# Kernel optimization log

Measured on AMD Instinct MI355X. Metric: run time of the kernel, lower is better.

Reference implementation:

```python
import jax, jax.numpy as jnp
import numpy as np

B, M, N = 2, 256, 256
K, P, Q, D = 8, 512, 512, 64
R, Pp, Qp, Dp = 128, 512, 512, 64
TEMP = float(np.sqrt(Dp))  # softmax temperature = sqrt(D')


def _xavier(key, shape):
    # xavier_uniform over last two dims (fan_in, fan_out), matching torch init on (K, d, D)
    fan_in, fan_out = shape[-2], shape[-1]
    lim = float(np.sqrt(6.0 / (fan_in + fan_out)))
    return jax.random.uniform(key, shape, jnp.float32, -lim, lim)


def setup_inputs() -> dict:
    key = jax.random.key(0)
    ks = jax.random.split(key, 9)
    return {
        "z": jax.random.normal(ks[0], (B, M, N, R), jnp.float32),
        "y_q": jax.random.normal(ks[1], (B, N, Qp), jnp.float32),
        "x_k": jax.random.normal(ks[2], (B, M, Pp), jnp.float32),
        "Theta_x": _xavier(ks[3], (K, P, D)),
        "Theta_y": _xavier(ks[4], (K, Q, D)),
        "Lam_x": _xavier(ks[5], (K, Pp, Dp)),
        "Lam_y": _xavier(ks[6], (K, Qp, Dp)),
        "Lam_zx": _xavier(ks[7], (K, R, Dp)),
        "Lam_zy": _xavier(ks[8], (K, R, Dp)),
    }


def reference(z, y_q, x_k, Theta_x, Theta_y, Lam_x, Lam_y, Lam_zx, Lam_zy):
    # --- mixed attention scores ---
    xt = jnp.einsum('bmp,kpd->bkmd', x_k, Lam_x)          # [B,K,M,D']
    yt = jnp.einsum('bnq,kqd->bknd', y_q, Lam_y)          # [B,K,N,D']
    r = jnp.einsum('bkmd,bknd->bkmn', xt, yt)             # pairwise term
    zy = jnp.einsum('bmnr,krd->bkmnd', z, Lam_zy)         # [B,K,M,N,D'] (large)
    r = r + jnp.einsum('bkmnd,bkmd->bkmn', zy, xt)
    r = r + jnp.einsum('bknd,bmnr,krd->bkmn', yt, z, Lam_zx)
    # --- generalised convolution (mask=None, bias=False) ---
    a = jax.nn.softmax(r / TEMP, axis=-2)                 # softmax over M (column-wise)
    xv = jnp.einsum('bmp,kpd->bkmd', x_k, Theta_x)        # value projection
    y = jnp.einsum('bkmn,bkmd,kqd->bnq', a, xv, Theta_y)  # [B,N,Q]
    return y
```

## Files before the change

### kernel.cpp

```cpp
#include <hip/hip_runtime.h>
#include <hip/hip_bf16.h>

#define LOG2E_OVER_T 0.18033688011112042f

typedef __attribute__((ext_vector_type(8))) short short8;
typedef __attribute__((ext_vector_type(4))) float f32x4;
typedef unsigned short ushort_t;
typedef unsigned long long ull_t;

#define MFMA16(a, b, c) __builtin_amdgcn_mfma_f32_16x16x32_bf16(a, b, c, 0, 0, 0)

__device__ __forceinline__ ushort_t f2bf(float f) {
    union { float f; unsigned u; } v; v.f = f;
    unsigned r = (v.u + 0x7fffu + ((v.u >> 16) & 1u)) >> 16;
    return (ushort_t)r;
}

__device__ __forceinline__ void split8(const float4 a, const float4 b,
                                       short8& hi, short8& lo)
{
    union { float f[8]; unsigned u[8]; } Z;
    Z.f[0] = a.x; Z.f[1] = a.y; Z.f[2] = a.z; Z.f[3] = a.w;
    Z.f[4] = b.x; Z.f[5] = b.y; Z.f[6] = b.z; Z.f[7] = b.w;
    union { unsigned u[4]; short8 s; } H, L;
    #pragma unroll
    for (int i = 0; i < 4; i++) {
        const unsigned u0 = Z.u[2 * i], u1 = Z.u[2 * i + 1];
        H.u[i] = __builtin_amdgcn_perm(u1, u0, 0x07060302u);
        union { unsigned u; float f; } h0, h1;
        h0.u = u0 & 0xffff0000u; h1.u = u1 & 0xffff0000u;
        union { float f; unsigned u; } l0, l1;
        l0.f = Z.f[2 * i] - h0.f; l1.f = Z.f[2 * i + 1] - h1.f;
        L.u[i] = __builtin_amdgcn_perm(l1.u, l0.u, 0x07060302u);
    }
    hi = H.s; lo = L.s;
}

__device__ __forceinline__ void mfma_core64(
    const ushort_t* __restrict__ Ag, int lda,
    const ushort_t* __restrict__ Btg, int ldb,
    int ksteps, f32x4 acc[2][2])
{
    __shared__ __align__(16) ushort_t As[64 * 40];
    __shared__ __align__(16) ushort_t Bs[64 * 40];
    const int t = threadIdx.x;
    const int srow = t >> 2, skc = (t & 3) * 8;
    const int lane = t & 63, w = t >> 6;
    const int wr = w >> 1, wc = w & 1;
    const int fr = lane & 15, kg = lane >> 4;
    const int aoff = (wr * 32 + fr) * 40 + kg * 8;
    const int boff = (wc * 32 + fr) * 40 + kg * 8;
    const long arow = (long)srow * lda + skc;
    const long brow = (long)srow * ldb + skc;

    short8 ra = *(const short8*)(Ag + arow);
    short8 rb = *(const short8*)(Btg + brow);
    for (int kt = 0; kt < ksteps; kt++) {
        __syncthreads();
        *(short8*)&As[srow * 40 + skc] = ra;
        *(short8*)&Bs[srow * 40 + skc] = rb;
        __syncthreads();
        if (kt + 1 < ksteps) {
            ra = *(const short8*)(Ag + arow + (kt + 1) * 32);
            rb = *(const short8*)(Btg + brow + (kt + 1) * 32);
        }
        short8 a0 = *(const short8*)&As[aoff];
        short8 a1 = *(const short8*)&As[aoff + 16 * 40];
        short8 b0 = *(const short8*)&Bs[boff];
        short8 b1 = *(const short8*)&Bs[boff + 16 * 40];
        acc[0][0] = MFMA16(a0, b0, acc[0][0]);
        acc[0][1] = MFMA16(a0, b1, acc[0][1]);
        acc[1][0] = MFMA16(a1, b0, acc[1][0]);
        acc[1][1] = MFMA16(a1, b1, acc[1][1]);
    }
}

__device__ __forceinline__ void zero_acc(f32x4 acc[2][2]) {
    const f32x4 z4 = {0.f, 0.f, 0.f, 0.f};
    acc[0][0] = z4; acc[0][1] = z4; acc[1][0] = z4; acc[1][1] = z4;
}

__global__ __launch_bounds__(256)
void convert_kernel(const float* __restrict__ x_k, const float* __restrict__ y_q,
                    const float* __restrict__ Lam_x, const float* __restrict__ Theta_x,
                    const float* __restrict__ Lam_y, const float* __restrict__ Lam_zy,
                    const float* __restrict__ Lam_zx, const float* __restrict__ Theta_y,
                    ushort_t* __restrict__ xkb, ushort_t* __restrict__ yqb,
                    ushort_t* __restrict__ WxTb, ushort_t* __restrict__ WyTb,
                    ushort_t* __restrict__ Zyb, ushort_t* __restrict__ Zxb,
                    ushort_t* __restrict__ TyTb, float* __restrict__ ssum)
{
    int i = blockIdx.x * 256 + threadIdx.x;
    if (i < 262144) { xkb[i] = f2bf(x_k[i]); return; }
    i -= 262144;
    if (i < 262144) { yqb[i] = f2bf(y_q[i]); return; }
    i -= 262144;
    if (i < 524288) {
        const int k = i >> 16, rem = i & 65535, dc = rem >> 9, p = i & 511;
        const float v = (dc < 64) ? Lam_x[((long)k * 512 + p) * 64 + dc]
                                  : Theta_x[((long)k * 512 + p) * 64 + dc - 64];
        WxTb[i] = f2bf(v); return;
    }
    i -= 524288;
    if (i < 262144) {
        const int k = i >> 15, d = (i >> 9) & 63, p = i & 511;
        WyTb[i] = f2bf(Lam_y[((long)k * 512 + p) * 64 + d]); return;
    }
    i -= 262144;
    if (i < 65536) { Zyb[i] = f2bf(Lam_zy[i]); return; }
    i -= 65536;
    if (i < 65536) { Zxb[i] = f2bf(Lam_zx[i]); return; }
    i -= 65536;
    if (i < 262144) {
        const int q = i >> 9, kd = i & 511, k = kd >> 6, d = kd & 63;
        TyTb[i] = f2bf(Theta_y[((long)k * 512 + q) * 64 + d]); return;
    }
    i -= 262144;
    ssum[i] = 0.f;
}

__global__ __launch_bounds__(256)
void proj_kernel(const ushort_t* __restrict__ xkb, const ushort_t* __restrict__ yqb,
                 const ushort_t* __restrict__ WxTb, const ushort_t* __restrict__ WyTb,
                 ushort_t* __restrict__ xtb, ushort_t* __restrict__ ytb,
                 ushort_t* __restrict__ xvTb)
{
    const int side = blockIdx.z;
    const int bx = blockIdx.x, by = blockIdx.y;
    if (side == 1 && bx >= 8) return;
    f32x4 acc[2][2]; zero_acc(acc);
    const int t = threadIdx.x, lane = t & 63, w = t >> 6;
    const int wr = w >> 1, wc = w & 1, fr = lane & 15, kg = lane >> 4;

    if (side == 0) {
        mfma_core64(xkb + (long)(by * 64) * 512, 512,
                    WxTb + (long)(bx * 64) * 512, 512, 16, acc);
        const int k = bx >> 1, isxv = bx & 1;
        #pragma unroll
        for (int mi = 0; mi < 2; mi++)
        #pragma unroll
        for (int ni = 0; ni < 2; ni++) {
            const int grow0 = by * 64 + wr * 32 + mi * 16 + kg * 4;
            const int b = grow0 >> 8, m0 = grow0 & 255;
            const int d = wc * 32 + ni * 16 + fr;
            if (!isxv) {
                #pragma unroll
                for (int j = 0; j < 4; j++)
                    xtb[(((long)(b * 8 + k)) * 256 + m0 + j) * 64 + d] = f2bf(acc[mi][ni][j]);
            } else {
                ull_t pk = (ull_t)f2bf(acc[mi][ni][0])
                         | ((ull_t)f2bf(acc[mi][ni][1]) << 16)
                         | ((ull_t)f2bf(acc[mi][ni][2]) << 32)
                         | ((ull_t)f2bf(acc[mi][ni][3]) << 48);
                *(ull_t*)&xvTb[(((long)(b * 8 + k)) * 64 + d) * 256 + m0] = pk;
            }
        }
    } else {
        mfma_core64(yqb + (long)(by * 64) * 512, 512,
                    WyTb + (long)(bx * 64) * 512, 512, 16, acc);
        const int k = bx;
        #pragma unroll
        for (int mi = 0; mi < 2; mi++)
        #pragma unroll
        for (int ni = 0; ni < 2; ni++)
        #pragma unroll
        for (int j = 0; j < 4; j++) {
            const int grow = by * 64 + wr * 32 + mi * 16 + kg * 4 + j;
            const int b = grow >> 8, n = grow & 255;
            const int d = wc * 32 + ni * 16 + fr;
            ytb[(((long)(b * 8 + k)) * 256 + n) * 64 + d] = f2bf(acc[mi][ni][j]);
        }
    }
}

__global__ __launch_bounds__(256)
void step2_kernel(const ushort_t* __restrict__ xtb, const ushort_t* __restrict__ ytb,
                  const ushort_t* __restrict__ Zyb, const ushort_t* __restrict__ Zxb,
                  ushort_t* __restrict__ wzyb, ushort_t* __restrict__ wzxb,
                  float* __restrict__ t1)
{
    const int bz = blockIdx.x;
    const int t = threadIdx.x, lane = t & 63, w = t >> 6;
    const int wr = w >> 1, wc = w & 1, fr = lane & 15, kg = lane >> 4;

    if (bz < 256) {
        const int which = bz >> 7, idx = bz & 127;
        const int bk = idx >> 3, tile = idx & 7, mt = tile >> 1, nt = tile & 1;
        const int k = bk & 7, b = bk >> 3;
        const ushort_t* Ag  = (which ? ytb : xtb) + ((long)bk * 256 + mt * 64) * 64;
        const ushort_t* Btg = (which ? Zxb : Zyb) + ((long)k * 128 + nt * 64) * 64;
        ushort_t* C = which ? wzxb : wzyb;
        f32x4 acc[2][2]; zero_acc(acc);
        mfma_core64(Ag, 64, Btg, 64, 2, acc);
        #pragma unroll
        for (int mi = 0; mi < 2; mi++)
        #pragma unroll
        for (int ni = 0; ni < 2; ni++)
        #pragma unroll
        for (int j = 0; j < 4; j++) {
            const int m_glob = mt * 64 + wr * 32 + mi * 16 + kg * 4 + j;
            const int r_glob = nt * 64 + wc * 32 + ni * 16 + fr;
            C[(((long)b * 256 + m_glob) * 8 + k) * 128 + r_glob] = f2bf(acc[mi][ni][j]);
        }
    } else {
        const int idx = bz - 256;
        const int bk = idx >> 4, tile = idx & 15, nt2 = tile >> 2, mt2 = tile & 3;
        f32x4 acc[2][2]; zero_acc(acc);
        mfma_core64(ytb + ((long)bk * 256 + nt2 * 64) * 64, 64,
                    xtb + ((long)bk * 256 + mt2 * 64) * 64, 64, 2, acc);
        #pragma unroll
        for (int mi = 0; mi < 2; mi++)
        #pragma unroll
        for (int ni = 0; ni < 2; ni++)
        #pragma unroll
        for (int j = 0; j < 4; j++) {
            const int n_glob = nt2 * 64 + wr * 32 + mi * 16 + kg * 4 + j;
            const int m_glob = mt2 * 64 + wc * 32 + ni * 16 + fr;
            t1[((long)bk * 256 + n_glob) * 256 + m_glob] = acc[mi][ni][j];
        }
    }
}

__global__ __launch_bounds__(256, 2)
void fused_score(const float* __restrict__ z,
                 const ushort_t* __restrict__ wzyb, const ushort_t* __restrict__ wzxb,
                 const float* __restrict__ t1, ushort_t* __restrict__ Et,
                 float* __restrict__ ssum)
{
    const int nt = blockIdx.x, mt = blockIdx.y, b = blockIdx.z;
    const int nbase = nt * 16, m0 = mt * 8;
    __shared__ float sc[4][8][8][17];

    const int tid = threadIdx.x;
    const int lane = tid & 63, w = tid >> 6;
    const int fr = lane & 15, kg = lane >> 4;
    const int f8 = fr & 7;
    const int rh = w * 32;

    {
        const float* zp = z + (((long)b * 256 + m0) * 256 + nbase + fr) * 128 + rh + kg * 8;
        const ushort_t* wp = wzyb + (((long)b * 256 + m0) * 8 + f8) * 128 + rh + kg * 8;
        float4 zA[8], zB[8]; short8 wv[8];
        #pragma unroll
        for (int m = 0; m < 8; m++) {
            zA[m] = *(const float4*)(zp + m * 32768);
            zB[m] = *(const float4*)(zp + m * 32768 + 4);
            wv[m] = *(const short8*)(wp + m * 1024);
        }
        __builtin_amdgcn_sched_barrier(0);
        #pragma unroll
        for (int m = 0; m < 8; m++) {
            short8 hi, lo;
            split8(zA[m], zB[m], hi, lo);
            f32x4 acc = {0.f, 0.f, 0.f, 0.f};
            acc = MFMA16(hi, wv[m], acc);
            acc = MFMA16(lo, wv[m], acc);
            if (fr < 8) {
                #pragma unroll
                for (int j = 0; j < 4; j++)
                    sc[w][m][fr][kg * 4 + j] = acc[j];
            }
        }
    }

    {
        const float* zp = z + (((long)b * 256 + m0 + f8) * 256 + nbase) * 128 + rh + kg * 8;
        const ushort_t* wp = wzxb + (((long)b * 256 + nbase) * 8 + f8) * 128 + rh + kg * 8;
        #pragma unroll
        for (int h = 0; h < 2; h++) {
            float4 zA[8], zB[8]; short8 wv[8];
            #pragma unroll
            for (int i = 0; i < 8; i++) {
                const int n = h * 8 + i;
                zA[i] = *(const float4*)(zp + n * 128);
                zB[i] = *(const float4*)(zp + n * 128 + 4);
                wv[i] = *(const short8*)(wp + n * 1024);
            }
            __builtin_amdgcn_sched_barrier(0);
            #pragma unroll
            for (int i = 0; i < 8; i++) {
                const int n = h * 8 + i;
                short8 hi, lo;
                split8(zA[i], zB[i], hi, lo);
                f32x4 acc = {0.f, 0.f, 0.f, 0.f};
                acc = MFMA16(hi, wv[i], acc);
                acc = MFMA16(lo, wv[i], acc);
                if (fr < 8 && kg < 2) {
                    #pragma unroll
                    for (int j = 0; j < 4; j++)
                        sc[w][kg * 4 + j][fr][n] += acc[j];
                }
            }
        }
    }
    __syncthreads();

    if (tid < 128) {
        const int k = tid >> 4, n = tid & 15;
        const float* tp = t1 + (((long)b * 8 + k) * 256 + nbase + n) * 256 + m0;
        const float4 t0 = *(const float4*)(tp);
        const float4 t4 = *(const float4*)(tp + 4);
        const float tv[8] = {t0.x, t0.y, t0.z, t0.w, t4.x, t4.y, t4.z, t4.w};
        float s8 = 0.f;
        ushort_t eb[8];
        #pragma unroll
        for (int m = 0; m < 8; m++) {
            const float s = sc[0][m][k][n] + sc[1][m][k][n]
                          + sc[2][m][k][n] + sc[3][m][k][n] + tv[m];
            const float e = exp2f(s * LOG2E_OVER_T);
            eb[m] = f2bf(e);
            s8 += e;
        }
        *(short8*)(Et + (((long)b * 8 + k) * 256 + nbase + n) * 256 + m0) = *(short8*)eb;
        atomicAdd(&ssum[(b * 8 + k) * 256 + nbase + n], s8);
    }
}

__global__ __launch_bounds__(256)
void ogemm_kernel(const ushort_t* __restrict__ Et, const ushort_t* __restrict__ xvTb,
                  const float* __restrict__ ssum, ushort_t* __restrict__ o2b)
{
    const int mt = blockIdx.x, bk = blockIdx.y;
    f32x4 acc[2][2]; zero_acc(acc);
    mfma_core64(Et + ((long)bk * 256 + mt * 64) * 256, 256,
                xvTb + (long)bk * 64 * 256, 256, 8, acc);
    const int t = threadIdx.x, lane = t & 63, w = t >> 6;
    const int wr = w >> 1, wc = w & 1, fr = lane & 15, kg = lane >> 4;
    const int b = bk >> 3, k = bk & 7;
    #pragma unroll
    for (int mi = 0; mi < 2; mi++)
    #pragma unroll
    for (int j = 0; j < 4; j++) {
        const int n = mt * 64 + wr * 32 + mi * 16 + kg * 4 + j;
        const float inv = 1.0f / ssum[bk * 256 + n];
        #pragma unroll
        for (int ni = 0; ni < 2; ni++) {
            const int d = wc * 32 + ni * 16 + fr;
            o2b[((long)b * 256 + n) * 512 + k * 64 + d] = f2bf(acc[mi][ni][j] * inv);
        }
    }
}

__global__ __launch_bounds__(256)
void ygemm_kernel(const ushort_t* __restrict__ o2b, const ushort_t* __restrict__ TyTb,
                  float* __restrict__ out)
{
    const int qt = blockIdx.x, mt = blockIdx.y, b = blockIdx.z;
    f32x4 acc[2][2]; zero_acc(acc);
    mfma_core64(o2b + ((long)b * 256 + mt * 64) * 512, 512,
                TyTb + (long)qt * 64 * 512, 512, 16, acc);
    const int t = threadIdx.x, lane = t & 63, w = t >> 6;
    const int wr = w >> 1, wc = w & 1, fr = lane & 15, kg = lane >> 4;
    #pragma unroll
    for (int mi = 0; mi < 2; mi++)
    #pragma unroll
    for (int ni = 0; ni < 2; ni++)
    #pragma unroll
    for (int j = 0; j < 4; j++) {
        const int n = mt * 64 + wr * 32 + mi * 16 + kg * 4 + j;
        const int q = qt * 64 + wc * 32 + ni * 16 + fr;
        out[((long)b * 256 + n) * 512 + q] = acc[mi][ni][j];
    }
}

extern "C" void kernel_launch(void* const* d_in, const int* in_sizes, int n_in,
                              void* d_out, int out_size, void* d_ws, size_t ws_size,
                              hipStream_t stream)
{
    const float* z       = (const float*)d_in[0];
    const float* y_q     = (const float*)d_in[1];
    const float* x_k     = (const float*)d_in[2];
    const float* Theta_x = (const float*)d_in[3];
    const float* Theta_y = (const float*)d_in[4];
    const float* Lam_x   = (const float*)d_in[5];
    const float* Lam_y   = (const float*)d_in[6];
    const float* Lam_zx  = (const float*)d_in[7];
    const float* Lam_zy  = (const float*)d_in[8];
    float* out = (float*)d_out;

    ushort_t* U = (ushort_t*)d_ws;
    ushort_t* xkb  = U;
    ushort_t* yqb  = U + 262144;
    ushort_t* WxTb = U + 524288;
    ushort_t* WyTb = U + 1048576;
    ushort_t* Zyb  = U + 1310720;
    ushort_t* Zxb  = U + 1376256;
    ushort_t* TyTb = U + 1441792;
    ushort_t* xtb  = U + 1703936;
    ushort_t* ytb  = U + 1966080;
    ushort_t* xvTb = U + 2228224;
    ushort_t* wzyb = U + 2490368;
    ushort_t* wzxb = U + 3014656;
    ushort_t* Et   = U + 3538944;
    ushort_t* o2b  = U + 4587520;
    float*    ssum = (float*)(U + 4849664);
    float*    t1   = (float*)(U + 4857856);

    convert_kernel<<<6672, 256, 0, stream>>>(x_k, y_q, Lam_x, Theta_x, Lam_y,
        Lam_zy, Lam_zx, Theta_y, xkb, yqb, WxTb, WyTb, Zyb, Zxb, TyTb, ssum);

    proj_kernel<<<dim3(16, 8, 2), 256, 0, stream>>>(xkb, yqb, WxTb, WyTb,
        xtb, ytb, xvTb);

    step2_kernel<<<512, 256, 0, stream>>>(xtb, ytb, Zyb, Zxb, wzyb, wzxb, t1);

    fused_score<<<dim3(16, 32, 2), 256, 0, stream>>>(z, wzyb, wzxb, t1,
        Et, ssum);

    ogemm_kernel<<<dim3(4, 16), 256, 0, stream>>>(Et, xvTb, ssum, o2b);

    ygemm_kernel<<<dim3(8, 4, 2), 256, 0, stream>>>(o2b, TyTb, out);
}
```

Before: 70.25 us.

## Stage z tiles in LDS via global_load_lds and share across both score terms

The fused score kernel now loads each 8x8x128 z chunk once into swizzled shared memory using direct global-to-LDS loads. Both the zy and zx contractions read from that staged tile, where before each read z from global memory separately. The aim is to halve global z traffic and cut register pressure, and the min-blocks launch bound is dropped. In exchange it adds two barriers per chunk, the tile is not double-buffered so load latency is exposed, and the first term now runs padded MFMAs with half the rows unused.

```diff
diff --git a/kernel.cpp b/kernel.cpp
--- a/kernel.cpp
+++ b/kernel.cpp
@@ -14,6 +14,12 @@
     union { float f; unsigned u; } v; v.f = f;
     unsigned r = (v.u + 0x7fffu + ((v.u >> 16) & 1u)) >> 16;
     return (ushort_t)r;
+}
+
+__device__ __forceinline__ void gload16(const float* g, float* l) {
+    __builtin_amdgcn_global_load_lds(
+        (const __attribute__((address_space(1))) void*)g,
+        (__attribute__((address_space(3))) void*)l, 16, 0, 0);
 }
 
 __device__ __forceinline__ void split8(const float4 a, const float4 b,
@@ -221,7 +227,7 @@
     }
 }
 
-__global__ __launch_bounds__(256, 2)
+__global__ __launch_bounds__(256)
 void fused_score(const float* __restrict__ z,
                  const ushort_t* __restrict__ wzyb, const ushort_t* __restrict__ wzxb,
                  const float* __restrict__ t1, ushort_t* __restrict__ Et,
@@ -229,71 +235,72 @@
 {
     const int nt = blockIdx.x, mt = blockIdx.y, b = blockIdx.z;
     const int nbase = nt * 16, m0 = mt * 8;
+    __shared__ __align__(16) float zs[8192];
     __shared__ float sc[4][8][8][17];
 
     const int tid = threadIdx.x;
     const int lane = tid & 63, w = tid >> 6;
     const int fr = lane & 15, kg = lane >> 4;
     const int f8 = fr & 7;
-    const int rh = w * 32;
-
-    {
-        const float* zp = z + (((long)b * 256 + m0) * 256 + nbase + fr) * 128 + rh + kg * 8;
-        const ushort_t* wp = wzyb + (((long)b * 256 + m0) * 8 + f8) * 128 + rh + kg * 8;
-        float4 zA[8], zB[8]; short8 wv[8];
+
+    const int js   = w * 512 + lane;
+    for (int c = 0; c < 2; c++) {
+        const int n0c = nbase + c * 8;
+
+        #pragma unroll
+        for (int i = 0; i < 8; i++) {
+            const int j   = js + i * 64;
+            const int row = j >> 5;
+            const int m_l = row >> 3, n_l = row & 7;
+            const int sl  = (j & 31) ^ ((m_l ^ n_l) & 7);
+            const float* src = z + (((long)b * 256 + m0 + m_l) * 256 + n0c + n_l) * 128 + sl * 4;
+            gload16(src, &zs[(w * 8 + i) * 256]);
+        }
+        __syncthreads();
+
         #pragma unroll
         for (int m = 0; m < 8; m++) {
-            zA[m] = *(const float4*)(zp + m * 32768);
-            zB[m] = *(const float4*)(zp + m * 32768 + 4);
-            wv[m] = *(const short8*)(wp + m * 1024);
-        }
-        __builtin_amdgcn_sched_barrier(0);
-        #pragma unroll
-        for (int m = 0; m < 8; m++) {
+            const int row = m * 8 + f8;
+            const int key = (m ^ f8) & 7;
+            const int s0 = (w * 8 + kg * 2) ^ key, s1 = (w * 8 + kg * 2 + 1) ^ key;
+            const float4 za = *(const float4*)&zs[row * 128 + s0 * 4];
+            const float4 zb = *(const float4*)&zs[row * 128 + s1 * 4];
+            const short8 wv = *(const short8*)(wzyb
+                + (((long)b * 256 + m0 + m) * 8 + f8) * 128 + w * 32 + kg * 8);
             short8 hi, lo;
-            split8(zA[m], zB[m], hi, lo);
+            split8(za, zb, hi, lo);
             f32x4 acc = {0.f, 0.f, 0.f, 0.f};
-            acc = MFMA16(hi, wv[m], acc);
-            acc = MFMA16(lo, wv[m], acc);
-            if (fr < 8) {
+            acc = MFMA16(hi, wv, acc);
+            acc = MFMA16(lo, wv, acc);
+            if (fr < 8 && kg < 2) {
                 #pragma unroll
                 for (int j = 0; j < 4; j++)
-                    sc[w][m][fr][kg * 4 + j] = acc[j];
+                    sc[w][m][fr][c * 8 + kg * 4 + j] = acc[j];
             }
         }
-    }
-
-    {
-        const float* zp = z + (((long)b * 256 + m0 + f8) * 256 + nbase) * 128 + rh + kg * 8;
-        const ushort_t* wp = wzxb + (((long)b * 256 + nbase) * 8 + f8) * 128 + rh + kg * 8;
-        #pragma unroll
-        for (int h = 0; h < 2; h++) {
-            float4 zA[8], zB[8]; short8 wv[8];
-            #pragma unroll
-            for (int i = 0; i < 8; i++) {
-                const int n = h * 8 + i;
-                zA[i] = *(const float4*)(zp + n * 128);
-                zB[i] = *(const float4*)(zp + n * 128 + 4);
-                wv[i] = *(const short8*)(wp + n * 1024);
+
+        #pragma unroll
+        for (int nl = 0; nl < 8; nl++) {
+            const int row = f8 * 8 + nl;
+            const int key = (f8 ^ nl) & 7;
+            const int s0 = (w * 8 + kg * 2) ^ key, s1 = (w * 8 + kg * 2 + 1) ^ key;
+            const float4 za = *(const float4*)&zs[row * 128 + s0 * 4];
+            const float4 zb = *(const float4*)&zs[row * 128 + s1 * 4];
+            const short8 wv = *(const short8*)(wzxb
+                + (((long)b * 256 + n0c + nl) * 8 + f8) * 128 + w * 32 + kg * 8);
+            short8 hi, lo;
+            split8(za, zb, hi, lo);
+            f32x4 acc = {0.f, 0.f, 0.f, 0.f};
+            acc = MFMA16(hi, wv, acc);
+            acc = MFMA16(lo, wv, acc);
+            if (fr < 8 && kg < 2) {
+                #pragma unroll
+                for (int j = 0; j < 4; j++)
+                    sc[w][kg * 4 + j][fr][c * 8 + nl] += acc[j];
             }
-            __builtin_amdgcn_sched_barrier(0);
-            #pragma unroll
-            for (int i = 0; i < 8; i++) {
-                const int n = h * 8 + i;
-                short8 hi, lo;
-                split8(zA[i], zB[i], hi, lo);
-                f32x4 acc = {0.f, 0.f, 0.f, 0.f};
-                acc = MFMA16(hi, wv[i], acc);
-                acc = MFMA16(lo, wv[i], acc);
-                if (fr < 8 && kg < 2) {
-                    #pragma unroll
-                    for (int j = 0; j < 4; j++)
-                        sc[w][kg * 4 + j][fr][n] += acc[j];
-                }
-            }
-        }
-    }
-    __syncthreads();
+        }
+        __syncthreads();
+    }
 
     if (tid < 128) {
         const int k = tid >> 4, n = tid & 15;
```

Result: faster. 58.93 us (-16.1%).
